# Performance work log

Measured on AMD Instinct MI355X. Metric: run time of the kernel, lower is better.

The kernel has to match this reference:

```python
import jax, jax.numpy as jnp
import numpy as np

N = 50000      # movie nodes
E = 1000000    # edges per metapath
F_IN = 512
HID = 128
HEADS = 8
D = HID // HEADS  # 16
OUT = 3
NEG_SLOPE = 0.2   # PyG HANConv leaky_relu slope


def setup_inputs() -> dict:
    key = jax.random.key(0)
    ks = jax.random.split(key, 16)
    x = jax.random.normal(ks[0], (N, F_IN), jnp.float32)
    ei0 = jax.random.randint(ks[1], (2, E), 0, N, jnp.int32)
    ei1 = jax.random.randint(ks[2], (2, E), 0, N, jnp.int32)
    W_proj = jax.random.normal(ks[3], (F_IN, HID), jnp.float32) / np.sqrt(F_IN)
    b_proj = jnp.zeros((HID,), jnp.float32)
    att_src0 = jax.random.normal(ks[4], (HEADS, D), jnp.float32) / np.sqrt(D)
    att_dst0 = jax.random.normal(ks[5], (HEADS, D), jnp.float32) / np.sqrt(D)
    att_src1 = jax.random.normal(ks[6], (HEADS, D), jnp.float32) / np.sqrt(D)
    att_dst1 = jax.random.normal(ks[7], (HEADS, D), jnp.float32) / np.sqrt(D)
    Wk = jax.random.normal(ks[8], (HID, HID), jnp.float32) / np.sqrt(HID)
    bk = jnp.zeros((HID,), jnp.float32)
    q = jax.random.normal(ks[9], (HID,), jnp.float32) / np.sqrt(HID)
    W_lin = jax.random.normal(ks[10], (HID, OUT), jnp.float32) / np.sqrt(HID)
    b_lin = jnp.zeros((OUT,), jnp.float32)
    return dict(x=x, edge_index_mp0=ei0, edge_index_mp1=ei1,
                W_proj=W_proj, b_proj=b_proj,
                att_src0=att_src0, att_dst0=att_dst0,
                att_src1=att_src1, att_dst1=att_dst1,
                Wk=Wk, bk=bk, q=q, W_lin=W_lin, b_lin=b_lin)


def _han_edge_type(xp, src, dst, att_src, att_dst):
    """Node-level multi-head attention for one metapath (eval mode, no dropout).
    xp: [N, H, D] projected features; src/dst: [E] indices.
    """
    a_src = jnp.einsum('nhd,hd->nh', xp, att_src)  # [N, H]
    a_dst = jnp.einsum('nhd,hd->nh', xp, att_dst)
    alpha = jax.nn.leaky_relu(a_src[src] + a_dst[dst], NEG_SLOPE)  # [E, H]
    # segment softmax over incoming edges of each dst node
    amax = jax.ops.segment_max(alpha, dst, num_segments=N)
    amax = jnp.where(jnp.isfinite(amax), amax, 0.0)
    ex = jnp.exp(alpha - amax[dst])
    denom = jax.ops.segment_sum(ex, dst, num_segments=N)
    w = ex / (denom[dst] + 1e-16)                 # [E, H]
    msg = w[:, :, None] * xp[src]                 # [E, H, D]
    out = jax.ops.segment_sum(msg, dst, num_segments=N)  # [N, H, D]
    return jax.nn.relu(out.reshape(N, HID))


def reference(x, edge_index_mp0, edge_index_mp1, W_proj, b_proj,
              att_src0, att_dst0, att_src1, att_dst1,
              Wk, bk, q, W_lin, b_lin):
    xp = (x @ W_proj + b_proj).reshape(N, HEADS, D)
    o0 = _han_edge_type(xp, edge_index_mp0[0], edge_index_mp0[1], att_src0, att_dst0)
    o1 = _han_edge_type(xp, edge_index_mp1[0], edge_index_mp1[1], att_src1, att_dst1)
    outs = jnp.stack([o0, o1], axis=0)            # [M=2, N, HID]
    # semantic-level attention: score_m = sum(q * mean_n tanh(k_lin(o_m)))
    scores = jnp.einsum('mh,h->m', jnp.tanh(outs @ Wk + bk).mean(axis=1), q)
    beta = jax.nn.softmax(scores)                 # [2]
    fused = jnp.einsum('m,mnh->nh', beta, outs)   # [N, HID]
    return fused @ W_lin + b_lin                  # [N, OUT]
```

## Files before the change

kernel.cpp:

```cpp
#include <hip/hip_runtime.h>
#include <hip/hip_bf16.h>

#define NN 50000
#define EE 1000000
#define FIN 512
#define HIDDEN 128
#define NH 8
#define DH 16
#define NOUT 3
#define NBUCK 196
#define EPB 8192
#define NBLKA ((EE + EPB - 1) / EPB)
#define ATTBLK ((NN*NH + 255) / 256)

typedef unsigned short u16;
typedef unsigned int u32;
typedef __attribute__((ext_vector_type(8))) short short8;
typedef __attribute__((ext_vector_type(4))) float f32x4;

__device__ __forceinline__ float b2f(u16 b) { return __uint_as_float(((u32)b) << 16); }
__device__ __forceinline__ u16 f2b(float f) { return (u16)(__float_as_uint(f) >> 16); }
__device__ __forceinline__ u16 f2b_rne(float f) {
    u32 u = __float_as_uint(f);
    return (u16)((u + 0x7FFFu + ((u >> 16) & 1u)) >> 16);
}

__device__ __forceinline__ void gload16(const u16* g, u16* l) {
    __builtin_amdgcn_global_load_lds(
        (const __attribute__((address_space(1))) unsigned int*)(g),
        (__attribute__((address_space(3))) unsigned int*)(l), 16, 0, 0);
}

#define W_BP   65536
#define W_AS0  65664
#define W_BK   82560
#define W_Q    82688
#define W_WL   82816
#define W_BL   83200

__global__ __launch_bounds__(256) void k_prep(
    const void* __restrict__ x, const void* __restrict__ Wp, const void* __restrict__ Wk,
    const void* bp, const void* as0, const void* ad0, const void* as1, const void* ad1,
    const void* bk, const void* q, const void* Wl, const void* bl,
    int* __restrict__ flag, float* __restrict__ scores, int* __restrict__ curA,
    float* __restrict__ wconv, u16* __restrict__ WhiT, u16* __restrict__ WloT,
    u16* __restrict__ WkThi)
{
    const int t = threadIdx.x;
    const int bid = blockIdx.x;

    const u16* xb = (const u16*)x;
    {
        float v = b2f(xb[((t*16 + (bid & 15))*131)*2]);
        float a = fabsf(v);
        int insane = ((a == 0.0f) || (a >= 1e-8f && a <= 1e4f)) ? 0 : 1;
        __shared__ int red[256];
        red[t] = insane;
        __syncthreads();
        for (int s = 128; s > 0; s >>= 1) { if (t < s) red[t] += red[t+s]; __syncthreads(); }
        const int f = (red[0] > 64) ? 1 : 0;
        if (bid == 0 && t == 0) { flag[0] = f; scores[0] = 0.f; scores[1] = 0.f; }

        if (bid < 256) {
            int idx = bid*256 + t;
            float w = f ? ((const float*)Wp)[idx] : b2f(((const u16*)Wp)[idx]);
            int k = idx >> 7, n = idx & 127;
            u32 hb = __float_as_uint(w) & 0xFFFF0000u;
            WhiT[(size_t)n*FIN + k] = (u16)(hb >> 16);
            WloT[(size_t)n*FIN + k] = f2b(w - __uint_as_float(hb));
        } else if (bid < 320) {
            int i = (bid-256)*256 + t;
            float w = f ? ((const float*)Wk)[i] : b2f(((const u16*)Wk)[i]);
            int k = i >> 7, h = i & 127;
            WkThi[(size_t)h*HIDDEN + k] = f2b_rne(w);
        } else if (bid == 320) {
            #pragma unroll
            for (int j = 0; j < 6; ++j) {
                int i = j*256 + t;
                if (i < 1283) {
                    const void* src; int off; int dst;
                    if (i < 640) {
                        dst = W_BP + i;
                        if (i < 128)      { src = bp;  off = i; }
                        else if (i < 256) { src = as0; off = i-128; }
                        else if (i < 384) { src = ad0; off = i-256; }
                        else if (i < 512) { src = as1; off = i-384; }
                        else              { src = ad1; off = i-512; }
                    } else if (i < 896) {
                        dst = W_BK + (i-640);
                        if (i < 768) { src = bk; off = i-640; }
                        else         { src = q;  off = i-768; }
                    } else {
                        dst = W_WL + (i-896);
                        if (i < 1280) { src = Wl; off = i-896; }
                        else          { src = bl; off = i-1280; }
                    }
                    wconv[dst] = f ? ((const float*)src)[off] : b2f(((const u16*)src)[off]);
                }
            }
        } else {
            int i = (bid-321)*256 + t;
            if (i < 8192) curA[i] = 0;
        }
    }
}

__global__ __launch_bounds__(256) void k_projm(
    const void* __restrict__ xv, const u16* __restrict__ WhiT,
    const u16* __restrict__ WloT, const float* __restrict__ bpf,
    const int* __restrict__ flag, u16* __restrict__ xpb)
{
    __shared__ u16 lds[2][16384];
    const int t = threadIdx.x;
    const int lane = t & 63;
    const int wid = t >> 6;
    const int m16 = lane & 15;
    const int quad = lane >> 4;
    const int wr = wid >> 1, wc = wid & 1;
    const int blockRow = blockIdx.x * 128;

    f32x4 acc[4][4];
    #pragma unroll
    for (int i = 0; i < 4; ++i)
        #pragma unroll
        for (int j = 0; j < 4; ++j) acc[i][j] = (f32x4)(0.f);

    if (flag[0]) {
        const float* xf = (const float*)xv;
        const int srow = t >> 1;
        const int shalf = t & 1;
        int gxrow = blockRow + srow; if (gxrow >= NN) gxrow = NN - 1;
        const float* xr = xf + (size_t)gxrow * FIN + shalf * 16;
        const int ssw = (srow >> 1) & 3;
        const int aw0 = srow*32 + ((shalf*2)     ^ ssw) * 8;
        const int aw1 = srow*32 + ((shalf*2 + 1) ^ ssw) * 8;

        int bp0 = t, bp1 = t + 256;
        int br0 = bp0 >> 2, br1 = bp1 >> 2;
        int bc0 = (bp0 & 3) ^ ((br0 >> 1) & 3);
        int bc1 = (bp1 & 3) ^ ((br1 >> 1) & 3);
        const u16* srcBh0 = WhiT + (size_t)br0 * FIN + bc0 * 8;
        const u16* srcBh1 = WhiT + (size_t)br1 * FIN + bc1 * 8;
        const u16* srcBl0 = WloT + (size_t)br0 * FIN + bc0 * 8;
        const u16* srcBl1 = WloT + (size_t)br1 * FIN + bc1 * 8;
        const int dB0 = bp0 * 8, dB1 = bp1 * 8;

        int aoff[4], boff[4];
        #pragma unroll
        for (int mt = 0; mt < 4; ++mt) {
            int r = wr*64 + mt*16 + m16;
            aoff[mt] = r*32 + ((quad ^ ((r >> 1) & 3)) << 3);
        }
        #pragma unroll
        for (int nt = 0; nt < 4; ++nt) {
            int r = wc*64 + nt*16 + m16;
            boff[nt] = r*32 + ((quad ^ ((r >> 1) & 3)) << 3);
        }

        u16* Lc = lds[0];
        u16* Ln = lds[1];
        {
            float4 v0 = *(const float4*)(xr);
            float4 v1 = *(const float4*)(xr + 4);
            float4 v2 = *(const float4*)(xr + 8);
            float4 v3 = *(const float4*)(xr + 12);
            gload16(srcBh0, Lc + 8192  + dB0);
            gload16(srcBh1, Lc + 8192  + dB1);
            gload16(srcBl0, Lc + 12288 + dB0);
            gload16(srcBl1, Lc + 12288 + dB1);
            float xs[16] = {v0.x,v0.y,v0.z,v0.w, v1.x,v1.y,v1.z,v1.w,
                            v2.x,v2.y,v2.z,v2.w, v3.x,v3.y,v3.z,v3.w};
            short8 h0, h1, l0, l1;
            #pragma unroll
            for (int j = 0; j < 8; ++j) {
                u32 u = __float_as_uint(xs[j]);   u32 hb = u & 0xFFFF0000u;
                h0[j] = (short)(hb >> 16); l0[j] = (short)f2b(xs[j] - __uint_as_float(hb));
                u32 u2 = __float_as_uint(xs[8+j]); u32 hb2 = u2 & 0xFFFF0000u;
                h1[j] = (short)(hb2 >> 16); l1[j] = (short)f2b(xs[8+j] - __uint_as_float(hb2));
            }
            *(short8*)(Lc + aw0) = h0;
            *(short8*)(Lc + aw1) = h1;
            *(short8*)(Lc + 4096 + aw0) = l0;
            *(short8*)(Lc + 4096 + aw1) = l1;
        }
        __syncthreads();

        #pragma unroll 1
        for (int ks = 0; ks < 16; ++ks) {
            const int kt = (ks + 1) * 32;
            float4 v0, v1, v2, v3;
            if (ks < 15) {
                v0 = *(const float4*)(xr + kt);
                v1 = *(const float4*)(xr + kt + 4);
                v2 = *(const float4*)(xr + kt + 8);
                v3 = *(const float4*)(xr + kt + 12);
                gload16(srcBh0 + kt, Ln + 8192  + dB0);
                gload16(srcBh1 + kt, Ln + 8192  + dB1);
                gload16(srcBl0 + kt, Ln + 12288 + dB0);
                gload16(srcBl1 + kt, Ln + 12288 + dB1);
            }
            short8 bh[4], bl[4];
            #pragma unroll
            for (int nt = 0; nt < 4; ++nt) {
                bh[nt] = *(const short8*)(Lc + 8192  + boff[nt]);
                bl[nt] = *(const short8*)(Lc + 12288 + boff[nt]);
            }
            #pragma unroll
            for (int mt = 0; mt < 4; ++mt) {
                short8 ah = *(const short8*)(Lc + aoff[mt]);
                short8 al = *(const short8*)(Lc + 4096 + aoff[mt]);
                #pragma unroll
                for (int nt = 0; nt < 4; ++nt) {
                    acc[mt][nt] = __builtin_amdgcn_mfma_f32_16x16x32_bf16(ah, bh[nt], acc[mt][nt], 0,0,0);
                    acc[mt][nt] = __builtin_amdgcn_mfma_f32_16x16x32_bf16(ah, bl[nt], acc[mt][nt], 0,0,0);
                    acc[mt][nt] = __builtin_amdgcn_mfma_f32_16x16x32_bf16(al, bh[nt], acc[mt][nt], 0,0,0);
                }
            }
            if (ks < 15) {
                float xs[16] = {v0.x,v0.y,v0.z,v0.w, v1.x,v1.y,v1.z,v1.w,
                                v2.x,v2.y,v2.z,v2.w, v3.x,v3.y,v3.z,v3.w};
                short8 h0, h1, l0, l1;
                #pragma unroll
                for (int j = 0; j < 8; ++j) {
                    u32 u = __float_as_uint(xs[j]);   u32 hb = u & 0xFFFF0000u;
                    h0[j] = (short)(hb >> 16); l0[j] = (short)f2b(xs[j] - __uint_as_float(hb));
                    u32 u2 = __float_as_uint(xs[8+j]); u32 hb2 = u2 & 0xFFFF0000u;
                    h1[j] = (short)(hb2 >> 16); l1[j] = (short)f2b(xs[8+j] - __uint_as_float(hb2));
                }
                *(short8*)(Ln + aw0) = h0;
                *(short8*)(Ln + aw1) = h1;
                *(short8*)(Ln + 4096 + aw0) = l0;
                *(short8*)(Ln + 4096 + aw1) = l1;
            }
            __syncthreads();
            u16* tmp = Lc; Lc = Ln; Ln = tmp;
        }
    } else {
        const u16* xb = (const u16*)xv;
        const int r0 = t >> 2,         c0 = (t & 3) * 8;
        const int r1 = (t + 256) >> 2, c1 = ((t + 256) & 3) * 8;
        int g0 = blockRow + r0; if (g0 >= NN) g0 = NN - 1;
        int g1 = blockRow + r1; if (g1 >= NN) g1 = NN - 1;
        const u16* srcA0  = xb   + (size_t)g0 * FIN + c0;
        const u16* srcA1  = xb   + (size_t)g1 * FIN + c1;
        const u16* srcBh0 = WhiT + (size_t)r0 * FIN + c0;
        const u16* srcBh1 = WhiT + (size_t)r1 * FIN + c1;
        const u16* srcBl0 = WloT + (size_t)r0 * FIN + c0;
        const u16* srcBl1 = WloT + (size_t)r1 * FIN + c1;

#define PSTAGE(buf, kt) do { \
        gload16(srcA0  + (kt), &lds[buf][t*8]); \
        gload16(srcA1  + (kt), &lds[buf][2048 + t*8]); \
        gload16(srcBh0 + (kt), &lds[buf][4096 + t*8]); \
        gload16(srcBh1 + (kt), &lds[buf][6144 + t*8]); \
        gload16(srcBl0 + (kt), &lds[buf][8192 + t*8]); \
        gload16(srcBl1 + (kt), &lds[buf][10240 + t*8]); \
    } while (0)

        PSTAGE(0, 0);
        __syncthreads();
        int cur = 0;
        for (int ks = 0; ks < 16; ++ks) {
            if (ks < 15) {
                if (cur) PSTAGE(0, (ks + 1) * 32);
                else     PSTAGE(1, (ks + 1) * 32);
            }
            const u16* L = lds[cur];
            short8 a[4], bh[4], bl[4];
            #pragma unroll
            for (int mt = 0; mt < 4; ++mt)
                a[mt] = *(const short8*)&L[(wr*64 + mt*16 + m16)*32 + quad*8];
            #pragma unroll
            for (int nt = 0; nt < 4; ++nt) {
                bh[nt] = *(const short8*)&L[4096 + (wc*64 + nt*16 + m16)*32 + quad*8];
                bl[nt] = *(const short8*)&L[8192 + (wc*64 + nt*16 + m16)*32 + quad*8];
            }
            #pragma unroll
            for (int mt = 0; mt < 4; ++mt)
                #pragma unroll
                for (int nt = 0; nt < 4; ++nt) {
                    acc[mt][nt] = __builtin_amdgcn_mfma_f32_16x16x32_bf16(a[mt], bh[nt], acc[mt][nt], 0,0,0);
                    acc[mt][nt] = __builtin_amdgcn_mfma_f32_16x16x32_bf16(a[mt], bl[nt], acc[mt][nt], 0,0,0);
                }
            __syncthreads();
            cur ^= 1;
        }
#undef PSTAGE
    }

    #pragma unroll
    for (int nt = 0; nt < 4; ++nt) {
        int col = wc*64 + nt*16 + m16;
        float bias = bpf[col];
        #pragma unroll
        for (int mt = 0; mt < 4; ++mt) {
            int orow0 = blockRow + wr*64 + mt*16 + quad*4;
            #pragma unroll
            for (int r = 0; r < 4; ++r) {
                int orow = orow0 + r;
                if (orow < NN) xpb[(size_t)orow*HIDDEN + col] = f2b_rne(acc[mt][nt][r] + bias);
            }
        }
    }
}

__global__ __launch_bounds__(256) void k_fused1(
    const u16* __restrict__ xpb, const float* __restrict__ watt,
    float* __restrict__ o_as0, float* __restrict__ o_ad0,
    float* __restrict__ o_as1, float* __restrict__ o_ad1,
    const int* __restrict__ ei0, const int* __restrict__ ei1,
    int* __restrict__ curA, u32* __restrict__ tmp0, u32* __restrict__ tmp1)
{
    __shared__ u32 ebuf[EPB];
    __shared__ int shA[256];
    __shared__ int shB[256];
    __shared__ int shC[256];
    __shared__ int shD[256];
    const int t = threadIdx.x;
    const int bid = blockIdx.x;

    if (bid < ATTBLK) {
        float* s0 = (float*)shA;
        float* d0 = s0 + 128;
        float* s1 = (float*)shB;
        float* d1 = s1 + 128;
        if (t < 128) { s0[t]=watt[t]; d0[t]=watt[128+t]; s1[t]=watt[256+t]; d1[t]=watt[384+t]; }
        __syncthreads();
        int tid = bid*256 + t;
        if (tid >= NN*NH) return;
        int h = tid & 7;
        const u32* px = (const u32*)(xpb + (size_t)tid * DH);
        float xv[16];
        #pragma unroll
        for (int i=0;i<8;++i){ u32 v=px[i]; xv[i*2]=b2f((u16)(v&0xFFFF)); xv[i*2+1]=b2f((u16)(v>>16)); }
        float r0=0.f,r1=0.f,r2=0.f,r3=0.f;
        #pragma unroll
        for (int d=0; d<16; ++d) {
            float xvd = xv[d];
            r0 += xvd*s0[h*16+d]; r1 += xvd*d0[h*16+d];
            r2 += xvd*s1[h*16+d]; r3 += xvd*d1[h*16+d];
        }
        o_as0[tid]=r0; o_ad0[tid]=r1; o_as1[tid]=r2; o_ad1[tid]=r3;
    } else {
        int r = bid - ATTBLK;
        const int mp = (r >= NBLKA) ? 1 : 0;
        const int bx = r - mp*NBLKA;
        const int* ei = mp ? ei1 : ei0;
        u32* tmp = mp ? tmp1 : tmp0;
        const int e0 = bx * EPB;
        const int wid = t >> 6, lane = t & 63;

        shA[t] = 0;
        __syncthreads();
        #pragma unroll
        for (int i = 0; i < EPB/256; ++i) {
            int idx = e0 + i*256 + t;
            if (idx < EE) atomicAdd(&shA[ei[EE + idx] >> 8], 1);
        }
        __syncthreads();
        int v = shA[t];
        shB[t] = v;
        __syncthreads();
        for (int off = 1; off < 256; off <<= 1) {
            int u = (t >= off) ? shB[t - off] : 0;
            __syncthreads();
            shB[t] += u;
            __syncthreads();
        }
        int excl = shB[t] - v;
        shB[t] = excl;
        shC[t] = 0;
        shD[t] = (t < NBUCK && v) ? atomicAdd(&curA[(mp*256 + t)*16], v) : 0;
        __syncthreads();
        #pragma unroll
        for (int i = 0; i < EPB/256; ++i) {
            int idx = e0 + i*256 + t;
            if (idx < EE) {
                int s = ei[idx], d = ei[EE + idx];
                int b = d >> 8;
                int pos = shB[b] + atomicAdd(&shC[b], 1);
                ebuf[pos] = (u32)(((d & 255) << 16) | s);
            }
        }
        __syncthreads();
        for (int b = wid; b < NBUCK; b += 4) {
            int h = shA[b];
            if (!h) continue;
            int lb = shB[b];
            u32 gb = ((u32)b << 13) + (u32)shD[b];
            for (int k = lane; k < h; k += 64)
                tmp[gb + k] = ebuf[lb + k];
        }
    }
}

__global__ __launch_bounds__(256) void k_scatterB(
    const u32* __restrict__ tmp0, const u32* __restrict__ tmp1,
    const int* __restrict__ bcap,
    int* __restrict__ ns0, int* __restrict__ ns1,
    int* __restrict__ nc0, int* __restrict__ nc1,
    u16* __restrict__ srt0, u16* __restrict__ srt1)
{
    const int b = blockIdx.x;
    const int mp = blockIdx.y;
    const u32* tmp = mp ? tmp1 : tmp0;
    int* nstart = mp ? ns1 : ns0;
    int* ncnt   = mp ? nc1 : nc0;
    u16* srt    = mp ? srt1 : srt0;
    const int cntb = bcap[(mp*256 + b)*16];
    const int segbase = b << 13;
    __shared__ u16 sl[EPB];
    __shared__ int lcnt[256];
    __shared__ int loff[256];
    const int t = threadIdx.x;
    lcnt[t] = 0;
    __syncthreads();
    for (int i = t; i < cntb; i += 256)
        atomicAdd(&lcnt[tmp[segbase + i] >> 16], 1);
    __syncthreads();
    int v = lcnt[t];
    loff[t] = v;
    __syncthreads();
    for (int off = 1; off < 256; off <<= 1) {
        int u = (t >= off) ? loff[t - off] : 0;
        __syncthreads();
        loff[t] += u;
        __syncthreads();
    }
    int excl = loff[t] - v;
    int node = (b << 8) + t;
    if (node < NN) { nstart[node] = segbase + excl; ncnt[node] = v; }
    __syncthreads();
    loff[t] = excl;
    lcnt[t] = 0;
    __syncthreads();
    for (int i = t; i < cntb; i += 256) {
        u32 p = tmp[segbase + i];
        int local = p >> 16;
        int pos = loff[local] + atomicAdd(&lcnt[local], 1);
        sl[pos] = (u16)(p & 0xFFFFu);
    }
    __syncthreads();
    for (int i = t; i < cntb; i += 256)
        srt[segbase + i] = sl[i];
}

__global__ __launch_bounds__(256) void k_gather(
    const u16* __restrict__ srt0, const u16* __restrict__ srt1,
    const int* __restrict__ ns0, const int* __restrict__ ns1,
    const int* __restrict__ nc0, const int* __restrict__ nc1,
    const float* __restrict__ as0, const float* __restrict__ ad0,
    const float* __restrict__ as1, const float* __restrict__ ad1,
    const u16* __restrict__ xpb, u16* __restrict__ obf0, u16* __restrict__ obf1)
{
    const int t = threadIdx.x;
    const int wid = blockIdx.x*4 + (t >> 6);
    if (wid >= NN) return;
    const int lane = t & 63;
    const int hc = lane & 7;
    const int eg = lane >> 3;
    const int mp = blockIdx.y;
    const u16*  srt  = mp ? srt1  : srt0;
    const int*  nstart = mp ? ns1 : ns0;
    const int*  ncnt   = mp ? nc1 : nc0;
    const float* asr = mp ? as1 : as0;
    const float* ads = mp ? ad1 : ad0;
    u16* obf = mp ? obf1 : obf0;
    const u32* xw = (const u32*)xpb;

    const int b = nstart[wid], e = b + ncnt[wid];
    const float adv = ads[wid*NH + hc];
    const int bp = (lane >> 3) << 2;
    float accx = 0.f, accy = 0.f, den = 0.f;

    for (int i = b; i < e; i += 8) {
        int il = i + eg;
        int ilc = il < e ? il : e - 1;
        int s = srt[ilc];

        u32 rv0, rv1, rv2, rv3, rv4, rv5, rv6, rv7;
        {
            const u32* r0p = xw + ((size_t)(u32)__builtin_amdgcn_readlane(s, 0)  << 6);
            const u32* r1p = xw + ((size_t)(u32)__builtin_amdgcn_readlane(s, 8)  << 6);
            const u32* r2p = xw + ((size_t)(u32)__builtin_amdgcn_readlane(s, 16) << 6);
            const u32* r3p = xw + ((size_t)(u32)__builtin_amdgcn_readlane(s, 24) << 6);
            const u32* r4p = xw + ((size_t)(u32)__builtin_amdgcn_readlane(s, 32) << 6);
            const u32* r5p = xw + ((size_t)(u32)__builtin_amdgcn_readlane(s, 40) << 6);
            const u32* r6p = xw + ((size_t)(u32)__builtin_amdgcn_readlane(s, 48) << 6);
            const u32* r7p = xw + ((size_t)(u32)__builtin_amdgcn_readlane(s, 56) << 6);
            rv0 = r0p[lane]; rv1 = r1p[lane]; rv2 = r2p[lane]; rv3 = r3p[lane];
            rv4 = r4p[lane]; rv5 = r5p[lane]; rv6 = r6p[lane]; rv7 = r7p[lane];
        }

        float av = asr[s*NH + hc] + adv;
        av = fmaxf(av, 0.2f*av);
        float w = (il < e) ? __expf(av) : 0.f;
        int wi = __float_as_int(w);

        #pragma unroll
        for (int k2 = 0; k2 < 8; ++k2) {
            float wk = __int_as_float(__builtin_amdgcn_ds_bpermute(bp + k2*32, wi));
            u32 v = (k2==0)?rv0:(k2==1)?rv1:(k2==2)?rv2:(k2==3)?rv3:
                    (k2==4)?rv4:(k2==5)?rv5:(k2==6)?rv6:rv7;
            accx = fmaf(wk, b2f((u16)(v & 0xFFFF)), accx);
            accy = fmaf(wk, b2f((u16)(v >> 16)), accy);
            den += wk;
        }
    }
    float inv = 1.f / (den + 1e-16f);
    u32 lo = f2b_rne(accx*inv), hi = f2b_rne(accy*inv);
    ((u32*)obf)[(size_t)wid*64 + lane] = (hi << 16) | lo;
}

__global__ __launch_bounds__(256) void k_semantic(
    const u16* __restrict__ obf0, const u16* __restrict__ obf1,
    const u16* __restrict__ WkThi, const float* __restrict__ bkf,
    const float* __restrict__ qf, float* __restrict__ scores)
{
    const int t = threadIdx.x;
    const int lane = t & 63;
    const int w = t >> 6;
    const int m16 = lane & 15;
    const int quad = lane >> 4;
    const int mp = blockIdx.y;
    const u16* om = mp ? obf1 : obf0;
    const int tile = blockIdx.x*4 + w;

    float partial = 0.f;
    if (tile < NN/16) {
        int row = tile*16 + m16;
        f32x4 acc[8];
        #pragma unroll
        for (int i=0;i<8;++i) acc[i] = (f32x4)(0.f);

        for (int kt = 0; kt < HIDDEN; kt += 32) {
            int kbase = kt + quad*8;
            short8 a = *(const short8*)(om + (size_t)row*HIDDEN + kbase);
            #pragma unroll
            for (int j=0;j<8;++j) a[j] = ((u16)a[j] & 0x8000u) ? (short)0 : a[j];
            #pragma unroll
            for (int nt = 0; nt < 8; ++nt) {
                int n = nt*16 + m16;
                short8 bhi = *(const short8*)(WkThi + (size_t)n*HIDDEN + kbase);
                acc[nt] = __builtin_amdgcn_mfma_f32_16x16x32_bf16(a, bhi, acc[nt], 0,0,0);
            }
        }
        #pragma unroll
        for (int nt=0; nt<8; ++nt) {
            int col = nt*16 + m16;
            float bkv = bkf[col], qv = qf[col];
            #pragma unroll
            for (int r=0;r<4;++r) {
                float xx = acc[nt][r] + bkv;
                xx = fminf(fmaxf(xx, -10.f), 10.f);
                float tex = __expf(2.f*xx);
                partial += qv * ((tex - 1.f) / (tex + 1.f));
            }
        }
    }
    __shared__ float red[256];
    red[t] = partial;
    __syncthreads();
    for (int s2 = 128; s2 > 0; s2 >>= 1) {
        if (t < s2) red[t] += red[t + s2];
        __syncthreads();
    }
    if (t == 0) unsafeAtomicAdd(&scores[mp], red[0]);
}

__global__ __launch_bounds__(256) void k_final(
    const u16* __restrict__ obf0, const u16* __restrict__ obf1,
    const float* __restrict__ scores, const float* __restrict__ Wlf,
    const float* __restrict__ blf, const int* __restrict__ flag,
    void* __restrict__ outv)
{
    __shared__ float fus[16*128];
    __shared__ float WlL[384];
    __shared__ float blL[3];
    const int t = threadIdx.x;
    for (int i = t; i < 384; i += 256) WlL[i] = Wlf[i];
    if (t < 3) blL[t] = blf[t];
    float sc0 = scores[0] / (float)NN;
    float sc1 = scores[1] / (float)NN;
    float m = fmaxf(sc0, sc1);
    float e0 = __expf(sc0-m), e1 = __expf(sc1-m);
    float binv = 1.f/(e0+e1);
    float b0 = e0*binv, b1 = e1*binv;

    const u32* o0w = (const u32*)obf0;
    const u32* o1w = (const u32*)obf1;
    size_t base = (size_t)blockIdx.x * 16 * 64;
    #pragma unroll
    for (int i=0;i<4;++i) {
        int j = t + i*256;
        u32 v0 = o0w[base + j];
        u32 v1 = o1w[base + j];
        float l0 = fmaxf(b2f((u16)(v0&0xFFFF)),0.f), h0 = fmaxf(b2f((u16)(v0>>16)),0.f);
        float l1 = fmaxf(b2f((u16)(v1&0xFFFF)),0.f), h1 = fmaxf(b2f((u16)(v1>>16)),0.f);
        int row = j >> 6, cp = j & 63;
        fus[row*128 + cp*2]     = b0*l0 + b1*l1;
        fus[row*128 + cp*2 + 1] = b0*h0 + b1*h1;
    }
    __syncthreads();
    if (t < 48) {
        int node = t / 3, c = t % 3;
        float acc = blL[c];
        const float* fr = &fus[node*128];
        #pragma unroll 16
        for (int k=0;k<128;++k) acc += fr[k]*WlL[k*3+c];
        size_t oi = (size_t)(blockIdx.x*16 + node)*NOUT + c;
        if (flag[0]) ((float*)outv)[oi] = acc;
        else         ((__hip_bfloat16*)outv)[oi] = __float2bfloat16(acc);
    }
}

extern "C" void kernel_launch(void* const* d_in, const int* in_sizes, int n_in,
                              void* d_out, int out_size, void* d_ws, size_t ws_size,
                              hipStream_t stream)
{
    const void* x   = d_in[0];
    const int* ei0  = (const int*)d_in[1];
    const int* ei1  = (const int*)d_in[2];

    float* ws = (float*)d_ws;
    u16*   xpb     = (u16*)ws;
    float* a_src0  = ws +  3200000;
    float* a_dst0  = ws +  3600000;
    float* a_src1  = ws +  4000000;
    float* a_dst1  = ws +  4400000;
    u16*   obf0    = (u16*)(ws + 4800000);
    u16*   obf1    = (u16*)(ws + 8000000);
    u16*   srt0    = (u16*)(ws + 11200000);
    u16*   srt1    = (u16*)(ws + 12810000);
    u32*   tmp0    = (u32*)(ws + 14420000);
    u32*   tmp1    = (u32*)(ws + 16030000);
    int*   nstart0 = (int*)(ws + 17640000);
    int*   nstart1 = (int*)(ws + 17690000);
    int*   ncnt0   = (int*)(ws + 17740000);
    int*   ncnt1   = (int*)(ws + 17790000);
    float* scores  = ws + 17840000;
    int*   flag    = (int*)(ws + 17840004);
    float* wconv   = ws + 17840008;
    int*   curA    = (int*)(ws + 17923216);
    u16*   WhiT    = (u16*)(ws + 17931408);
    u16*   WloT    = (u16*)(ws + 17964176);
    u16*   WkThi   = (u16*)(ws + 17996944);

    k_prep<<<353, 256, 0, stream>>>(
        x, d_in[3], d_in[9], d_in[4], d_in[5], d_in[6], d_in[7], d_in[8],
        d_in[10], d_in[11], d_in[12], d_in[13],
        flag, scores, curA, wconv, WhiT, WloT, WkThi);

    k_projm<<<(NN+127)/128, 256, 0, stream>>>(x, WhiT, WloT, wconv + W_BP, flag, xpb);

    k_fused1<<<ATTBLK + 2*NBLKA, 256, 0, stream>>>(
        xpb, wconv + W_AS0, a_src0, a_dst0, a_src1, a_dst1,
        ei0, ei1, curA, tmp0, tmp1);

    k_scatterB<<<dim3(NBUCK,2), 256, 0, stream>>>(
        tmp0, tmp1, curA, nstart0, nstart1, ncnt0, ncnt1, srt0, srt1);

    k_gather<<<dim3((NN + 3)/4, 2), 256, 0, stream>>>(
        srt0, srt1, nstart0, nstart1, ncnt0, ncnt1,
        a_src0, a_dst0, a_src1, a_dst1, xpb, obf0, obf1);

    k_semantic<<<dim3((NN/16 + 3)/4, 2), 256, 0, stream>>>(
        obf0, obf1, WkThi, wconv + W_BK, wconv + W_Q, scores);

    k_final<<<NN/16, 256, 0, stream>>>(obf0, obf1, scores, wconv + W_WL, wconv + W_BL,
                                       flag, d_out);
}
```

Before: 396.2 us.

## Co-schedule edge bucketing with projection GEMM and attention with node sort

Moves the edge-bucketing pass (stage A) into the projection GEMM launch as extra blocks, and merges the per-node attention-score computation with the second-stage bucket sort into one launch. Independent work now runs concurrently inside each launch, and one kernel launch and its dependency barrier go away. The bucketing blocks now carry the GEMM's 64KB LDS allocation, which may lower their occupancy, and the blocks in each launch become more heterogeneous.

```diff
diff --git a/kernel.cpp b/kernel.cpp
--- a/kernel.cpp
+++ b/kernel.cpp
@@ -11,6 +11,7 @@
 #define NBUCK 196
 #define EPB 8192
 #define NBLKA ((EE + EPB - 1) / EPB)
+#define PROJBLK ((NN + 127) / 128)
 #define ATTBLK ((NN*NH + 255) / 256)
 
 typedef unsigned short u16;
@@ -105,15 +106,76 @@
     }
 }
 
-__global__ __launch_bounds__(256) void k_projm(
+__global__ __launch_bounds__(256) void k_projm_sa(
     const void* __restrict__ xv, const u16* __restrict__ WhiT,
     const u16* __restrict__ WloT, const float* __restrict__ bpf,
-    const int* __restrict__ flag, u16* __restrict__ xpb)
+    const int* __restrict__ flag, u16* __restrict__ xpb,
+    const int* __restrict__ ei0, const int* __restrict__ ei1,
+    int* __restrict__ curA, u32* __restrict__ tmp0, u32* __restrict__ tmp1)
 {
     __shared__ u16 lds[2][16384];
     const int t = threadIdx.x;
     const int lane = t & 63;
     const int wid = t >> 6;
+
+    if (blockIdx.x >= PROJBLK) {
+        int r = blockIdx.x - PROJBLK;
+        const int mp = (r >= NBLKA) ? 1 : 0;
+        const int bx = r - mp*NBLKA;
+        const int* ei = mp ? ei1 : ei0;
+        u32* tmp = mp ? tmp1 : tmp0;
+        const int e0 = bx * EPB;
+        u32* ebuf = (u32*)&lds[0][0];
+        int* shA  = (int*)(&lds[0][0] + 16384);
+        int* shB  = shA + 256;
+        int* shC  = shB + 256;
+        int* shD  = shC + 256;
+
+        shA[t] = 0;
+        __syncthreads();
+        #pragma unroll
+        for (int i = 0; i < EPB/256; ++i) {
+            int idx = e0 + i*256 + t;
+            if (idx < EE) atomicAdd(&shA[ei[EE + idx] >> 8], 1);
+        }
+        __syncthreads();
+        int v = shA[t];
+        shB[t] = v;
+        __syncthreads();
+        for (int off = 1; off < 256; off <<= 1) {
+            int u = (t >= off) ? shB[t - off] : 0;
+            __syncthreads();
+            shB[t] += u;
+            __syncthreads();
+        }
+        int excl = shB[t] - v;
+        __syncthreads();
+        shB[t] = excl;
+        shC[t] = 0;
+        shD[t] = (t < NBUCK && v) ? atomicAdd(&curA[(mp*256 + t)*16], v) : 0;
+        __syncthreads();
+        #pragma unroll
+        for (int i = 0; i < EPB/256; ++i) {
+            int idx = e0 + i*256 + t;
+            if (idx < EE) {
+                int s = ei[idx], d = ei[EE + idx];
+                int b = d >> 8;
+                int pos = shB[b] + atomicAdd(&shC[b], 1);
+                ebuf[pos] = (u32)(((d & 255) << 16) | s);
+            }
+        }
+        __syncthreads();
+        for (int b = wid; b < NBUCK; b += 4) {
+            int h = shA[b];
+            if (!h) continue;
+            int lb = shB[b];
+            u32 gb = ((u32)b << 13) + (u32)shD[b];
+            for (int k = lane; k < h; k += 64)
+                tmp[gb + k] = ebuf[lb + k];
+        }
+        return;
+    }
+
     const int m16 = lane & 15;
     const int quad = lane >> 4;
     const int wr = wid >> 1, wc = wid & 1;
@@ -148,13 +210,13 @@
         int aoff[4], boff[4];
         #pragma unroll
         for (int mt = 0; mt < 4; ++mt) {
-            int r = wr*64 + mt*16 + m16;
-            aoff[mt] = r*32 + ((quad ^ ((r >> 1) & 3)) << 3);
+            int rr = wr*64 + mt*16 + m16;
+            aoff[mt] = rr*32 + ((quad ^ ((rr >> 1) & 3)) << 3);
         }
         #pragma unroll
         for (int nt = 0; nt < 4; ++nt) {
-            int r = wc*64 + nt*16 + m16;
-            boff[nt] = r*32 + ((quad ^ ((r >> 1) & 3)) << 3);
+            int rr = wc*64 + nt*16 + m16;
+            boff[nt] = rr*32 + ((quad ^ ((rr >> 1) & 3)) << 3);
         }
 
         u16* Lc = lds[0];
@@ -233,7 +295,7 @@
                 *(short8*)(Ln + 4096 + aw1) = l1;
             }
             __syncthreads();
-            u16* tmp = Lc; Lc = Ln; Ln = tmp;
+            u16* tmp2 = Lc; Lc = Ln; Ln = tmp2;
         }
     } else {
         const u16* xb = (const u16*)xv;
@@ -304,145 +366,85 @@
     }
 }
 
-__global__ __launch_bounds__(256) void k_fused1(
+__global__ __launch_bounds__(256) void k_att_sb(
     const u16* __restrict__ xpb, const float* __restrict__ watt,
     float* __restrict__ o_as0, float* __restrict__ o_ad0,
     float* __restrict__ o_as1, float* __restrict__ o_ad1,
-    const int* __restrict__ ei0, const int* __restrict__ ei1,
-    int* __restrict__ curA, u32* __restrict__ tmp0, u32* __restrict__ tmp1)
-{
-    __shared__ u32 ebuf[EPB];
-    __shared__ int shA[256];
-    __shared__ int shB[256];
-    __shared__ int shC[256];
-    __shared__ int shD[256];
-    const int t = threadIdx.x;
-    const int bid = blockIdx.x;
-
-    if (bid < ATTBLK) {
-        float* s0 = (float*)shA;
-        float* d0 = s0 + 128;
-        float* s1 = (float*)shB;
-        float* d1 = s1 + 128;
-        if (t < 128) { s0[t]=watt[t]; d0[t]=watt[128+t]; s1[t]=watt[256+t]; d1[t]=watt[384+t]; }
-        __syncthreads();
-        int tid = bid*256 + t;
-        if (tid >= NN*NH) return;
-        int h = tid & 7;
-        const u32* px = (const u32*)(xpb + (size_t)tid * DH);
-        float xv[16];
-        #pragma unroll
-        for (int i=0;i<8;++i){ u32 v=px[i]; xv[i*2]=b2f((u16)(v&0xFFFF)); xv[i*2+1]=b2f((u16)(v>>16)); }
-        float r0=0.f,r1=0.f,r2=0.f,r3=0.f;
-        #pragma unroll
-        for (int d=0; d<16; ++d) {
-            float xvd = xv[d];
-            r0 += xvd*s0[h*16+d]; r1 += xvd*d0[h*16+d];
-            r2 += xvd*s1[h*16+d]; r3 += xvd*d1[h*16+d];
-        }
-        o_as0[tid]=r0; o_ad0[tid]=r1; o_as1[tid]=r2; o_ad1[tid]=r3;
-    } else {
-        int r = bid - ATTBLK;
-        const int mp = (r >= NBLKA) ? 1 : 0;
-        const int bx = r - mp*NBLKA;
-        const int* ei = mp ? ei1 : ei0;
-        u32* tmp = mp ? tmp1 : tmp0;
-        const int e0 = bx * EPB;
-        const int wid = t >> 6, lane = t & 63;
-
-        shA[t] = 0;
-        __syncthreads();
-        #pragma unroll
-        for (int i = 0; i < EPB/256; ++i) {
-            int idx = e0 + i*256 + t;
-            if (idx < EE) atomicAdd(&shA[ei[EE + idx] >> 8], 1);
-        }
-        __syncthreads();
-        int v = shA[t];
-        shB[t] = v;
-        __syncthreads();
-        for (int off = 1; off < 256; off <<= 1) {
-            int u = (t >= off) ? shB[t - off] : 0;
-            __syncthreads();
-            shB[t] += u;
-            __syncthreads();
-        }
-        int excl = shB[t] - v;
-        shB[t] = excl;
-        shC[t] = 0;
-        shD[t] = (t < NBUCK && v) ? atomicAdd(&curA[(mp*256 + t)*16], v) : 0;
-        __syncthreads();
-        #pragma unroll
-        for (int i = 0; i < EPB/256; ++i) {
-            int idx = e0 + i*256 + t;
-            if (idx < EE) {
-                int s = ei[idx], d = ei[EE + idx];
-                int b = d >> 8;
-                int pos = shB[b] + atomicAdd(&shC[b], 1);
-                ebuf[pos] = (u32)(((d & 255) << 16) | s);
-            }
-        }
-        __syncthreads();
-        for (int b = wid; b < NBUCK; b += 4) {
-            int h = shA[b];
-            if (!h) continue;
-            int lb = shB[b];
-            u32 gb = ((u32)b << 13) + (u32)shD[b];
-            for (int k = lane; k < h; k += 64)
-                tmp[gb + k] = ebuf[lb + k];
-        }
-    }
-}
-
-__global__ __launch_bounds__(256) void k_scatterB(
     const u32* __restrict__ tmp0, const u32* __restrict__ tmp1,
     const int* __restrict__ bcap,
     int* __restrict__ ns0, int* __restrict__ ns1,
     int* __restrict__ nc0, int* __restrict__ nc1,
     u16* __restrict__ srt0, u16* __restrict__ srt1)
 {
-    const int b = blockIdx.x;
-    const int mp = blockIdx.y;
-    const u32* tmp = mp ? tmp1 : tmp0;
-    int* nstart = mp ? ns1 : ns0;
-    int* ncnt   = mp ? nc1 : nc0;
-    u16* srt    = mp ? srt1 : srt0;
-    const int cntb = bcap[(mp*256 + b)*16];
-    const int segbase = b << 13;
-    __shared__ u16 sl[EPB];
-    __shared__ int lcnt[256];
-    __shared__ int loff[256];
+    __shared__ u16 sh3[9216];
     const int t = threadIdx.x;
-    lcnt[t] = 0;
-    __syncthreads();
-    for (int i = t; i < cntb; i += 256)
-        atomicAdd(&lcnt[tmp[segbase + i] >> 16], 1);
-    __syncthreads();
-    int v = lcnt[t];
-    loff[t] = v;
-    __syncthreads();
-    for (int off = 1; off < 256; off <<= 1) {
-        int u = (t >= off) ? loff[t - off] : 0;
-        __syncthreads();
-        loff[t] += u;
-        __syncthreads();
-    }
-    int excl = loff[t] - v;
-    int node = (b << 8) + t;
-    if (node < NN) { nstart[node] = segbase + excl; ncnt[node] = v; }
-    __syncthreads();
-    loff[t] = excl;
-    lcnt[t] = 0;
-    __syncthreads();
-    for (int i = t; i < cntb; i += 256) {
-        u32 p = tmp[segbase + i];
-        int local = p >> 16;
-        int pos = loff[local] + atomicAdd(&lcnt[local], 1);
-        sl[pos] = (u16)(p & 0xFFFFu);
-    }
-    __syncthreads();
-    for (int i = t; i < cntb; i += 256)
-        srt[segbase + i] = sl[i];
+    const int bid = blockIdx.x;
+
+    if (bid < 2*NBUCK) {
+        const int mp = (bid >= NBUCK) ? 1 : 0;
+        const int b = bid - mp*NBUCK;
+        const u32* tmp = mp ? tmp1 : tmp0;
+        int* nstart = mp ? ns1 : ns0;
+        int* ncnt   = mp ? nc1 : nc0;
+        u16* srt    = mp ? srt1 : srt0;
+        const int cntb = bcap[(mp*256 + b)*16];
+        const int segbase = b << 13;
+        u16* sl   = sh3;
+        int* lcnt = (int*)(sh3 + 8192);
+        int* loff = lcnt + 256;
+        lcnt[t] = 0;
+        __syncthreads();
+        for (int i = t; i < cntb; i += 256)
+            atomicAdd(&lcnt[tmp[segbase + i] >> 16], 1);
+        __syncthreads();
+        int v = lcnt[t];
+        loff[t] = v;
+        __syncthreads();
+        for (int off = 1; off < 256; off <<= 1) {
+            int u = (t >= off) ? loff[t - off] : 0;
+            __syncthreads();
+            loff[t] += u;
+            __syncthreads();
+        }
+        int excl = loff[t] - v;
+        int node = (b << 8) + t;
+        if (node < NN) { nstart[node] = segbase + excl; ncnt[node] = v; }
+        __syncthreads();
+        loff[t] = excl;
+        lcnt[t] = 0;
+        __syncthreads();
+        for (int i = t; i < cntb; i += 256) {
+            u32 p = tmp[segbase + i];
+            int local = p >> 16;
+            int pos = loff[local] + atomicAdd(&lcnt[local], 1);
+            sl[pos] = (u16)(p & 0xFFFFu);
+        }
+        __syncthreads();
+        for (int i = t; i < cntb; i += 256)
+            srt[segbase + i] = sl[i];
+    } else {
+        float* s0 = (float*)sh3;
+        float* d0 = s0 + 128;
+        float* s1 = s0 + 256;
+        float* d1 = s0 + 384;
+        if (t < 128) { s0[t]=watt[t]; d0[t]=watt[128+t]; s1[t]=watt[256+t]; d1[t]=watt[384+t]; }
+        __syncthreads();
+        int tid = (bid - 2*NBUCK)*256 + t;
+        if (tid >= NN*NH) return;
+        int h = tid & 7;
+        const u32* px = (const u32*)(xpb + (size_t)tid * DH);
+        float xv[16];
+        #pragma unroll
+        for (int i=0;i<8;++i){ u32 v=px[i]; xv[i*2]=b2f((u16)(v&0xFFFF)); xv[i*2+1]=b2f((u16)(v>>16)); }
+        float r0=0.f,r1=0.f,r2=0.f,r3=0.f;
+        #pragma unroll
+        for (int d=0; d<16; ++d) {
+            float xvd = xv[d];
+            r0 += xvd*s0[h*16+d]; r1 += xvd*d0[h*16+d];
+            r2 += xvd*s1[h*16+d]; r3 += xvd*d1[h*16+d];
+        }
+        o_as0[tid]=r0; o_ad0[tid]=r1; o_as1[tid]=r2; o_ad1[tid]=r3;
+    }
 }
 
 __global__ __launch_bounds__(256) void k_gather(
@@ -651,13 +653,12 @@
         d_in[10], d_in[11], d_in[12], d_in[13],
         flag, scores, curA, wconv, WhiT, WloT, WkThi);
 
-    k_projm<<<(NN+127)/128, 256, 0, stream>>>(x, WhiT, WloT, wconv + W_BP, flag, xpb);
-
-    k_fused1<<<ATTBLK + 2*NBLKA, 256, 0, stream>>>(
+    k_projm_sa<<<PROJBLK + 2*NBLKA, 256, 0, stream>>>(
+        x, WhiT, WloT, wconv + W_BP, flag, xpb,
+        ei0, ei1, curA, tmp0, tmp1);
+
+    k_att_sb<<<2*NBUCK + ATTBLK, 256, 0, stream>>>(
         xpb, wconv + W_AS0, a_src0, a_dst0, a_src1, a_dst1,
-        ei0, ei1, curA, tmp0, tmp1);
-
-    k_scatterB<<<dim3(NBUCK,2), 256, 0, stream>>>(
         tmp0, tmp1, curA, nstart0, nstart1, ncnt0, ncnt1, srt0, srt1);
 
     k_gather<<<dim3((NN + 3)/4, 2), 256, 0, stream>>>(
```

New measurement: 389.3 us. No clear change (-1.7%).
